# Kernel optimization log

Hardware: AMD Instinct MI355X
Metric: run time of the kernel (lower is better)

## Reference

```python
import jax, jax.numpy as jnp
import numpy as np

N, D, E, H, K = 4096, 512, 32, 128, 4  # tokens, d_model, n_experts, expert hidden, top-k


def setup_inputs() -> dict:
    key = jax.random.key(0)
    k0, k1, k2, k3 = jax.random.split(key, 4)
    x = jax.random.normal(k0, (N, D), dtype=jnp.float32)
    # router weights, init std = d**-0.5 (matches get_initializer std)
    expert_sel = jax.random.normal(k1, (E, D), dtype=jnp.float32) * (D ** -0.5)
    # per-expert MLP weights (Linear stores [out, in]; we keep [E, in, out] layout)
    w1 = jax.random.normal(k2, (E, D, H), dtype=jnp.float32) * (D ** -0.5)
    w2 = jax.random.normal(k3, (E, H, D), dtype=jnp.float32) * (H ** -0.5)
    return {"x": x, "expert_sel": expert_sel, "w1": w1, "w2": w2}


def reference(x, expert_sel, w1, w2):
    # routing: sigmoid selection, top-k experts per token
    scores = jax.nn.sigmoid(x @ expert_sel.T)          # [N, E]
    gate_vals, gate_idx = jax.lax.top_k(scores, K)     # [N, K]
    # dense gate matrix with only top-k nonzero (sparse dispatch/combine weights)
    gate = (jax.nn.one_hot(gate_idx, E, dtype=x.dtype) * gate_vals[..., None]).sum(-2)  # [N, E]
    # per-expert MLP; gating at hidden is exact since experts have no bias:
    # gate * (relu(x W1) W2) == (gate * relu(x W1)) W2
    h = jax.nn.relu(jnp.einsum('nd,edh->neh', x, w1)) * gate[..., None]  # [N, E, H]
    y = jnp.einsum('neh,ehv->nv', h, w2)               # [N, D]
    return y
```

## Files before the change

### kernel.cpp

```cpp
#include <hip/hip_runtime.h>
#include <hip/hip_bf16.h>

#define NTOK 4096
#define DM   512
#define NE   32
#define HD   128
#define TK   4

typedef unsigned short u16;
typedef unsigned int   u32;
typedef u16   u16x4 __attribute__((ext_vector_type(4)));
typedef u16   u16x8 __attribute__((ext_vector_type(8)));
typedef short short8 __attribute__((ext_vector_type(8)));
typedef float f32x4 __attribute__((ext_vector_type(4)));

__device__ __forceinline__ u16 f2bf(float f) {
    union { float f; u32 u; } v; v.f = f;
    return (u16)((v.u + 0x7FFFu + ((v.u >> 16) & 1u)) >> 16);
}
__device__ __forceinline__ float bf2f(u16 h) {
    union { u32 u; float f; } v; v.u = ((u32)h) << 16; return v.f;
}

__global__ __launch_bounds__(256) void prep_kernel(const float* __restrict__ x,
                                                   const float* __restrict__ sel,
                                                   const float* __restrict__ w1,
                                                   const float* __restrict__ w2,
                                                   int* __restrict__ counts_pad,
                                                   int* __restrict__ tok_list,
                                                   float* __restrict__ gate_list,
                                                   u16* __restrict__ xbf,
                                                   u16* __restrict__ wf1,
                                                   u16* __restrict__ wf2) {
    __shared__ float  xs[4][520];
    __shared__ double sc[4][33];
    int tid = threadIdx.x;
    int wv = tid >> 6, lane = tid & 63;

    if (blockIdx.x >= 1024) {
        int m = lane & 15, q = lane >> 4;
        int f0 = ((blockIdx.x - 1024) * 4 + wv) * 2;
        const float* in[2]; u16* outp[2]; int Nd[2];
#pragma unroll
        for (int u = 0; u < 2; ++u) {
            int w = f0 + u;
            if (w < 4096) {
                int e = w >> 7, rem = w & 127, ks = rem >> 3, nt = rem & 7;
                in[u] = w1 + (size_t)e * DM * HD + (size_t)(32 * ks + q * 8) * HD + 16 * nt + m;
                Nd[u] = HD;
                outp[u] = wf1 + (size_t)w * 512 + lane * 8;
            } else {
                int wl = w - 4096, e = wl >> 7, rem = wl & 127, ks = rem >> 5, nt = rem & 31;
                in[u] = w2 + (size_t)e * HD * DM + (size_t)(32 * ks + q * 8) * DM + 16 * nt + m;
                Nd[u] = DM;
                outp[u] = wf2 + (size_t)wl * 512 + lane * 8;
            }
        }
        float v[2][8];
#pragma unroll
        for (int u = 0; u < 2; ++u)
#pragma unroll
            for (int j = 0; j < 8; ++j) v[u][j] = in[u][(size_t)j * Nd[u]];
#pragma unroll
        for (int u = 0; u < 2; ++u) {
            u16x8 h;
#pragma unroll
            for (int j = 0; j < 8; ++j) h[j] = f2bf(v[u][j]);
            *(u16x8*)outp[u] = h;
        }
        return;
    }

    int tb = blockIdx.x * 4;
#pragma unroll
    for (int rep = 0; rep < 2; ++rep) {
        int idx = (rep * 256 + tid) * 4;
        int row = idx >> 9, col = idx & 511;
        f32x4 v = *(const f32x4*)(x + (size_t)(tb + row) * DM + col);
        *(f32x4*)&xs[row][col] = v;
        u16x4 h;
#pragma unroll
        for (int j = 0; j < 4; ++j) h[j] = f2bf(v[j]);
        *(u16x4*)(xbf + (size_t)(tb + row) * DM + col) = h;
    }
    __syncthreads();

    int tok = tid & 3, seg = (tid >> 2) & 1, e = tid >> 3;
    const float* sp = sel + (size_t)e * DM + seg * 256;
    const float* xp = &xs[tok][seg * 256];
    double pa = 0.0, pb = 0.0, pc = 0.0, pd = 0.0;
#pragma unroll 4
    for (int j = 0; j < 256; j += 16) {
        f32x4 x0 = *(const f32x4*)(xp + j);
        f32x4 x1 = *(const f32x4*)(xp + j + 4);
        f32x4 x2 = *(const f32x4*)(xp + j + 8);
        f32x4 x3 = *(const f32x4*)(xp + j + 12);
        f32x4 s0 = *(const f32x4*)(sp + j);
        f32x4 s1 = *(const f32x4*)(sp + j + 4);
        f32x4 s2 = *(const f32x4*)(sp + j + 8);
        f32x4 s3 = *(const f32x4*)(sp + j + 12);
#pragma unroll
        for (int k = 0; k < 4; ++k) {
            pa = fma((double)x0[k], (double)s0[k], pa);
            pb = fma((double)x1[k], (double)s1[k], pb);
            pc = fma((double)x2[k], (double)s2[k], pc);
            pd = fma((double)x3[k], (double)s3[k], pd);
        }
    }
    double p = (pa + pb) + (pc + pd);
    p += __shfl_xor(p, 4);
    if (seg == 0) sc[tok][e] = p;
    __syncthreads();

    if (tid < 4) {
        int t = tb + tid;
        unsigned mask = 0;
        for (int k = 0; k < TK; ++k) {
            double best = -1e300; int be = 0;
            for (int ee = 0; ee < NE; ++ee) {
                double v = sc[tid][ee];
                if (!((mask >> ee) & 1u) && v > best) { best = v; be = ee; }
            }
            mask |= 1u << be;
            float gate = 1.0f / (1.0f + __expf(-(float)best));
            int pos = atomicAdd(&counts_pad[32 * be], 1);
            tok_list[be * NTOK + pos]  = (k << 16) | t;
            gate_list[be * NTOK + pos] = gate;
        }
    }
}

__global__ __launch_bounds__(256, 2) void moe_mlp_kernel(const u16* __restrict__ xbf,
                                                         const u16* __restrict__ wf1,
                                                         const u16* __restrict__ wf2,
                                                         const int* __restrict__ counts_pad,
                                                         const int* __restrict__ tok_list,
                                                         const float* __restrict__ gate_list,
                                                         u16* __restrict__ part,
                                                         float* __restrict__ out,
                                                         int use_part) {
    __shared__ int   s_cnt[NE];
    __shared__ int   s_ent[64];
    __shared__ float s_gate[64];
    __shared__ __align__(16) u16 Hm[64][136];
    __shared__ __align__(16) u16 Ct[32][520];

    int tid = threadIdx.x;
    if (tid < NE) s_cnt[tid] = counts_pad[32 * tid];
    __syncthreads();

    int b = blockIdx.x;
    int xcd = b & 7, idx = b >> 3;
    int e = -1, t = 0, rows = 0, pre = 0;
#pragma unroll
    for (int j = 0; j < 4; ++j) {
        int ee = xcd + 8 * j;
        int cc = s_cnt[ee];
        int nt = (cc + 63) >> 6;
        if (e < 0 && idx < pre + nt) { e = ee; t = idx - pre; rows = cc - t * 64; if (rows > 64) rows = 64; }
        pre += nt;
    }
    if (e < 0) return;

    if (tid < 64) {
        int base = e * NTOK + t * 64;
        bool val = tid < rows;
        s_ent[tid]  = tok_list[base + (val ? tid : 0)];
        s_gate[tid] = val ? gate_list[base + tid] : 0.0f;
    }
    __syncthreads();

    int wv = tid >> 6, lane = tid & 63, m = lane & 15, q = lane >> 4;
    int r = wv >> 1, c = wv & 1;
    const u16* w1f = wf1 + (size_t)e * (128 * 512);
    const u16* w2f = wf2 + (size_t)e * (128 * 512);

    const u16* a0 = xbf + (size_t)(s_ent[32 * r + m] & 0xFFFF) * DM + q * 8;
    const u16* a1 = xbf + (size_t)(s_ent[32 * r + 16 + m] & 0xFFFF) * DM + q * 8;

    short8 ab[2][2][2];
    short8 bb[2][2][4];
#pragma unroll
    for (int kk = 0; kk < 2; ++kk) {
        ab[0][kk][0] = *(const short8*)(a0 + 32 * kk);
        ab[0][kk][1] = *(const short8*)(a1 + 32 * kk);
        const u16* bp = w1f + (size_t)kk * 4096 + (size_t)(4 * c) * 512 + lane * 8;
#pragma unroll
        for (int n = 0; n < 4; ++n) bb[0][kk][n] = *(const short8*)(bp + n * 512);
    }
    f32x4 acc[2][4];
#pragma unroll
    for (int i = 0; i < 2; ++i)
#pragma unroll
        for (int n = 0; n < 4; ++n) acc[i][n] = (f32x4){0.f, 0.f, 0.f, 0.f};

#pragma unroll
    for (int kp = 0; kp < 8; ++kp) {
        int cur = kp & 1, nxt = cur ^ 1;
        if (kp < 7) {
            int ks0 = 2 * (kp + 1);
#pragma unroll
            for (int kk = 0; kk < 2; ++kk) {
                ab[nxt][kk][0] = *(const short8*)(a0 + 32 * (ks0 + kk));
                ab[nxt][kk][1] = *(const short8*)(a1 + 32 * (ks0 + kk));
                const u16* bp = w1f + (size_t)(ks0 + kk) * 4096 + (size_t)(4 * c) * 512 + lane * 8;
#pragma unroll
                for (int n = 0; n < 4; ++n) bb[nxt][kk][n] = *(const short8*)(bp + n * 512);
            }
        }
#pragma unroll
        for (int kk = 0; kk < 2; ++kk)
#pragma unroll
            for (int i = 0; i < 2; ++i)
#pragma unroll
                for (int n = 0; n < 4; ++n)
                    acc[i][n] = __builtin_amdgcn_mfma_f32_16x16x32_bf16(ab[cur][kk][i],
                                                                        bb[cur][kk][n],
                                                                        acc[i][n], 0, 0, 0);
    }

#pragma unroll
    for (int i = 0; i < 2; ++i) {
        int rb = 32 * r + 16 * i + q * 4;
#pragma unroll
        for (int n = 0; n < 4; ++n)
#pragma unroll
            for (int rr = 0; rr < 4; ++rr)
                Hm[rb + rr][64 * c + 16 * n + m] =
                    f2bf(fmaxf(acc[i][n][rr], 0.f) * s_gate[rb + rr]);
    }

    short8 cb[4][8];
#pragma unroll
    for (int ks = 0; ks < 4; ++ks) {
        const u16* bp = w2f + (size_t)(ks * 32 + wv * 8) * 512 + lane * 8;
#pragma unroll
        for (int n = 0; n < 8; ++n) cb[ks][n] = *(const short8*)(bp + n * 512);
    }
    __syncthreads();

#pragma unroll
    for (int half = 0; half < 2; ++half) {
        f32x4 acc2[2][8];
#pragma unroll
        for (int i = 0; i < 2; ++i)
#pragma unroll
            for (int n = 0; n < 8; ++n) acc2[i][n] = (f32x4){0.f, 0.f, 0.f, 0.f};
#pragma unroll
        for (int ks = 0; ks < 4; ++ks) {
            short8 h0 = *(const short8*)&Hm[32 * half + m][32 * ks + q * 8];
            short8 h1 = *(const short8*)&Hm[32 * half + 16 + m][32 * ks + q * 8];
#pragma unroll
            for (int n = 0; n < 8; ++n) {
                acc2[0][n] = __builtin_amdgcn_mfma_f32_16x16x32_bf16(h0, cb[ks][n], acc2[0][n], 0, 0, 0);
                acc2[1][n] = __builtin_amdgcn_mfma_f32_16x16x32_bf16(h1, cb[ks][n], acc2[1][n], 0, 0, 0);
            }
        }
#pragma unroll
        for (int i = 0; i < 2; ++i) {
            int rb = 16 * i + q * 4;
#pragma unroll
            for (int n = 0; n < 8; ++n)
#pragma unroll
                for (int rr = 0; rr < 4; ++rr)
                    Ct[rb + rr][128 * wv + 16 * n + m] = f2bf(acc2[i][n][rr]);
        }
        __syncthreads();
#pragma unroll
        for (int rep = 0; rep < 8; ++rep) {
            int rl = rep * 4 + wv;
            int rt = 32 * half + rl;
            u16x8 v = *(const u16x8*)&Ct[rl][lane * 8];
            if (rt < rows) {
                int en = s_ent[rt];
                int tk = en & 0xFFFF, sl2 = en >> 16;
                if (use_part) {
                    *(u16x8*)(part + ((size_t)sl2 * NTOK + tk) * DM + lane * 8) = v;
                } else {
                    float* op = out + (size_t)tk * DM + lane * 8;
#pragma unroll
                    for (int j = 0; j < 8; ++j) atomicAdd(&op[j], bf2f(v[j]));
                }
            }
        }
        __syncthreads();
    }
}

__global__ __launch_bounds__(256) void combine_kernel(const u16* __restrict__ part,
                                                      float* __restrict__ out) {
    size_t off = ((size_t)blockIdx.x * 256 + threadIdx.x) * 8;
    float s[8] = {0, 0, 0, 0, 0, 0, 0, 0};
#pragma unroll
    for (int k = 0; k < TK; ++k) {
        u16x8 p = *(const u16x8*)(part + (size_t)k * NTOK * DM + off);
#pragma unroll
        for (int j = 0; j < 8; ++j) s[j] += bf2f(p[j]);
    }
    *(f32x4*)(out + off)     = (f32x4){s[0], s[1], s[2], s[3]};
    *(f32x4*)(out + off + 4) = (f32x4){s[4], s[5], s[6], s[7]};
}

extern "C" void kernel_launch(void* const* d_in, const int* in_sizes, int n_in,
                              void* d_out, int out_size, void* d_ws, size_t ws_size,
                              hipStream_t stream) {
    const float* x   = (const float*)d_in[0];
    const float* sel = (const float*)d_in[1];
    const float* w1  = (const float*)d_in[2];
    const float* w2  = (const float*)d_in[3];
    float* out = (float*)d_out;

    char* ws = (char*)d_ws;
    int*   counts_pad = (int*)(ws);
    int*   tok_list   = (int*)(ws + 4096);
    float* gate_list  = (float*)(ws + 4096 + (size_t)NE * NTOK * 4);
    u16*   xbf  = (u16*)(ws + 4096 + (size_t)NE * NTOK * 8);
    u16*   wf1  = xbf + (size_t)NTOK * DM;
    u16*   wf2  = wf1 + (size_t)NE * HD * DM;
    u16*   part = wf2 + (size_t)NE * HD * DM;

    size_t need = 4096 + (size_t)NE * NTOK * 8 + (size_t)NTOK * DM * 2
                + 2 * (size_t)NE * HD * DM * 2 + (size_t)TK * NTOK * DM * 2;
    int use_part = (ws_size >= need) ? 1 : 0;

    hipMemsetAsync(counts_pad, 0, 4096, stream);
    if (!use_part)
        hipMemsetAsync(d_out, 0, (size_t)NTOK * DM * sizeof(float), stream);

    prep_kernel<<<2048, 256, 0, stream>>>(x, sel, w1, w2, counts_pad, tok_list,
                                          gate_list, xbf, wf1, wf2);
    moe_mlp_kernel<<<2080, 256, 0, stream>>>(xbf, wf1, wf2, counts_pad, tok_list,
                                             gate_list, part, out, use_part);
    if (use_part)
        combine_kernel<<<NTOK * DM / 8 / 256, 256, 0, stream>>>(part, out);
}
```

Baseline: 120.5 us.

## Halve MoE token tile to 32 rows and double-buffer W2 loads

Each block of the expert MLP kernel now handles 32 routed tokens instead of 64, and the grid doubles to 4096 blocks. The goal is less padding waste per expert and more blocks to spread across CUs. The second GEMM now streams W2 fragments through a two-slot register buffer instead of preloading all four k-slices, which cuts register pressure. In exchange, each expert's W1/W2 weights are reloaded twice as often per token, so global weight traffic rises.

```diff
diff --git a/kernel.cpp b/kernel.cpp
--- a/kernel.cpp
+++ b/kernel.cpp
@@ -140,9 +140,9 @@
                                                          float* __restrict__ out,
                                                          int use_part) {
     __shared__ int   s_cnt[NE];
-    __shared__ int   s_ent[64];
-    __shared__ float s_gate[64];
-    __shared__ __align__(16) u16 Hm[64][136];
+    __shared__ int   s_ent[32];
+    __shared__ float s_gate[32];
+    __shared__ __align__(16) u16 Hm[32][136];
     __shared__ __align__(16) u16 Ct[32][520];
 
     int tid = threadIdx.x;
@@ -156,14 +156,14 @@
     for (int j = 0; j < 4; ++j) {
         int ee = xcd + 8 * j;
         int cc = s_cnt[ee];
-        int nt = (cc + 63) >> 6;
-        if (e < 0 && idx < pre + nt) { e = ee; t = idx - pre; rows = cc - t * 64; if (rows > 64) rows = 64; }
+        int nt = (cc + 31) >> 5;
+        if (e < 0 && idx < pre + nt) { e = ee; t = idx - pre; rows = cc - t * 32; if (rows > 32) rows = 32; }
         pre += nt;
     }
     if (e < 0) return;
 
-    if (tid < 64) {
-        int base = e * NTOK + t * 64;
+    if (tid < 32) {
+        int base = e * NTOK + t * 32;
         bool val = tid < rows;
         s_ent[tid]  = tok_list[base + (val ? tid : 0)];
         s_gate[tid] = val ? gate_list[base + tid] : 0.0f;
@@ -175,24 +175,20 @@
     const u16* w1f = wf1 + (size_t)e * (128 * 512);
     const u16* w2f = wf2 + (size_t)e * (128 * 512);
 
-    const u16* a0 = xbf + (size_t)(s_ent[32 * r + m] & 0xFFFF) * DM + q * 8;
-    const u16* a1 = xbf + (size_t)(s_ent[32 * r + 16 + m] & 0xFFFF) * DM + q * 8;
-
-    short8 ab[2][2][2];
+    const u16* a0 = xbf + (size_t)(s_ent[16 * r + m] & 0xFFFF) * DM + q * 8;
+
+    short8 ab[2][2];
     short8 bb[2][2][4];
 #pragma unroll
     for (int kk = 0; kk < 2; ++kk) {
-        ab[0][kk][0] = *(const short8*)(a0 + 32 * kk);
-        ab[0][kk][1] = *(const short8*)(a1 + 32 * kk);
+        ab[0][kk] = *(const short8*)(a0 + 32 * kk);
         const u16* bp = w1f + (size_t)kk * 4096 + (size_t)(4 * c) * 512 + lane * 8;
 #pragma unroll
         for (int n = 0; n < 4; ++n) bb[0][kk][n] = *(const short8*)(bp + n * 512);
     }
-    f32x4 acc[2][4];
-#pragma unroll
-    for (int i = 0; i < 2; ++i)
-#pragma unroll
-        for (int n = 0; n < 4; ++n) acc[i][n] = (f32x4){0.f, 0.f, 0.f, 0.f};
+    f32x4 acc[4];
+#pragma unroll
+    for (int n = 0; n < 4; ++n) acc[n] = (f32x4){0.f, 0.f, 0.f, 0.f};
 
 #pragma unroll
     for (int kp = 0; kp < 8; ++kp) {
@@ -201,8 +197,7 @@
             int ks0 = 2 * (kp + 1);
 #pragma unroll
             for (int kk = 0; kk < 2; ++kk) {
-                ab[nxt][kk][0] = *(const short8*)(a0 + 32 * (ks0 + kk));
-                ab[nxt][kk][1] = *(const short8*)(a1 + 32 * (ks0 + kk));
+                ab[nxt][kk] = *(const short8*)(a0 + 32 * (ks0 + kk));
                 const u16* bp = w1f + (size_t)(ks0 + kk) * 4096 + (size_t)(4 * c) * 512 + lane * 8;
 #pragma unroll
                 for (int n = 0; n < 4; ++n) bb[nxt][kk][n] = *(const short8*)(bp + n * 512);
@@ -211,79 +206,77 @@
 #pragma unroll
         for (int kk = 0; kk < 2; ++kk)
 #pragma unroll
-            for (int i = 0; i < 2; ++i)
-#pragma unroll
-                for (int n = 0; n < 4; ++n)
-                    acc[i][n] = __builtin_amdgcn_mfma_f32_16x16x32_bf16(ab[cur][kk][i],
-                                                                        bb[cur][kk][n],
-                                                                        acc[i][n], 0, 0, 0);
-    }
-
-#pragma unroll
-    for (int i = 0; i < 2; ++i) {
-        int rb = 32 * r + 16 * i + q * 4;
+            for (int n = 0; n < 4; ++n)
+                acc[n] = __builtin_amdgcn_mfma_f32_16x16x32_bf16(ab[cur][kk],
+                                                                 bb[cur][kk][n],
+                                                                 acc[n], 0, 0, 0);
+    }
+
+    {
+        int rb = 16 * r + q * 4;
 #pragma unroll
         for (int n = 0; n < 4; ++n)
 #pragma unroll
             for (int rr = 0; rr < 4; ++rr)
                 Hm[rb + rr][64 * c + 16 * n + m] =
-                    f2bf(fmaxf(acc[i][n][rr], 0.f) * s_gate[rb + rr]);
-    }
-
-    short8 cb[4][8];
+                    f2bf(fmaxf(acc[n][rr], 0.f) * s_gate[rb + rr]);
+    }
+
+    short8 cb[2][8];
+    {
+        const u16* bp = w2f + (size_t)(wv * 8) * 512 + lane * 8;
+#pragma unroll
+        for (int n = 0; n < 8; ++n) cb[0][n] = *(const short8*)(bp + n * 512);
+    }
+    __syncthreads();
+
+    f32x4 acc2[2][8];
+#pragma unroll
+    for (int i = 0; i < 2; ++i)
+#pragma unroll
+        for (int n = 0; n < 8; ++n) acc2[i][n] = (f32x4){0.f, 0.f, 0.f, 0.f};
 #pragma unroll
     for (int ks = 0; ks < 4; ++ks) {
-        const u16* bp = w2f + (size_t)(ks * 32 + wv * 8) * 512 + lane * 8;
-#pragma unroll
-        for (int n = 0; n < 8; ++n) cb[ks][n] = *(const short8*)(bp + n * 512);
-    }
-    __syncthreads();
-
-#pragma unroll
-    for (int half = 0; half < 2; ++half) {
-        f32x4 acc2[2][8];
-#pragma unroll
-        for (int i = 0; i < 2; ++i)
-#pragma unroll
-            for (int n = 0; n < 8; ++n) acc2[i][n] = (f32x4){0.f, 0.f, 0.f, 0.f};
-#pragma unroll
-        for (int ks = 0; ks < 4; ++ks) {
-            short8 h0 = *(const short8*)&Hm[32 * half + m][32 * ks + q * 8];
-            short8 h1 = *(const short8*)&Hm[32 * half + 16 + m][32 * ks + q * 8];
-#pragma unroll
-            for (int n = 0; n < 8; ++n) {
-                acc2[0][n] = __builtin_amdgcn_mfma_f32_16x16x32_bf16(h0, cb[ks][n], acc2[0][n], 0, 0, 0);
-                acc2[1][n] = __builtin_amdgcn_mfma_f32_16x16x32_bf16(h1, cb[ks][n], acc2[1][n], 0, 0, 0);
+        int cur = ks & 1, nxt = cur ^ 1;
+        if (ks < 3) {
+            const u16* bp = w2f + (size_t)((ks + 1) * 32 + wv * 8) * 512 + lane * 8;
+#pragma unroll
+            for (int n = 0; n < 8; ++n) cb[nxt][n] = *(const short8*)(bp + n * 512);
+        }
+        short8 h0 = *(const short8*)&Hm[m][32 * ks + q * 8];
+        short8 h1 = *(const short8*)&Hm[16 + m][32 * ks + q * 8];
+#pragma unroll
+        for (int n = 0; n < 8; ++n) {
+            acc2[0][n] = __builtin_amdgcn_mfma_f32_16x16x32_bf16(h0, cb[cur][n], acc2[0][n], 0, 0, 0);
+            acc2[1][n] = __builtin_amdgcn_mfma_f32_16x16x32_bf16(h1, cb[cur][n], acc2[1][n], 0, 0, 0);
+        }
+    }
+
+#pragma unroll
+    for (int i = 0; i < 2; ++i) {
+        int rb = 16 * i + q * 4;
+#pragma unroll
+        for (int n = 0; n < 8; ++n)
+#pragma unroll
+            for (int rr = 0; rr < 4; ++rr)
+                Ct[rb + rr][128 * wv + 16 * n + m] = f2bf(acc2[i][n][rr]);
+    }
+    __syncthreads();
+#pragma unroll
+    for (int rep = 0; rep < 8; ++rep) {
+        int rl = rep * 4 + wv;
+        u16x8 v = *(const u16x8*)&Ct[rl][lane * 8];
+        if (rl < rows) {
+            int en = s_ent[rl];
+            int tk = en & 0xFFFF, sl2 = en >> 16;
+            if (use_part) {
+                *(u16x8*)(part + ((size_t)sl2 * NTOK + tk) * DM + lane * 8) = v;
+            } else {
+                float* op = out + (size_t)tk * DM + lane * 8;
+#pragma unroll
+                for (int j = 0; j < 8; ++j) atomicAdd(&op[j], bf2f(v[j]));
             }
         }
-#pragma unroll
-        for (int i = 0; i < 2; ++i) {
-            int rb = 16 * i + q * 4;
-#pragma unroll
-            for (int n = 0; n < 8; ++n)
-#pragma unroll
-                for (int rr = 0; rr < 4; ++rr)
-                    Ct[rb + rr][128 * wv + 16 * n + m] = f2bf(acc2[i][n][rr]);
-        }
-        __syncthreads();
-#pragma unroll
-        for (int rep = 0; rep < 8; ++rep) {
-            int rl = rep * 4 + wv;
-            int rt = 32 * half + rl;
-            u16x8 v = *(const u16x8*)&Ct[rl][lane * 8];
-            if (rt < rows) {
-                int en = s_ent[rt];
-                int tk = en & 0xFFFF, sl2 = en >> 16;
-                if (use_part) {
-                    *(u16x8*)(part + ((size_t)sl2 * NTOK + tk) * DM + lane * 8) = v;
-                } else {
-                    float* op = out + (size_t)tk * DM + lane * 8;
-#pragma unroll
-                    for (int j = 0; j < 8; ++j) atomicAdd(&op[j], bf2f(v[j]));
-                }
-            }
-        }
-        __syncthreads();
     }
 }
 
@@ -329,7 +322,7 @@
 
     prep_kernel<<<2048, 256, 0, stream>>>(x, sel, w1, w2, counts_pad, tok_list,
                                           gate_list, xbf, wf1, wf2);
-    moe_mlp_kernel<<<2080, 256, 0, stream>>>(xbf, wf1, wf2, counts_pad, tok_list,
+    moe_mlp_kernel<<<4096, 256, 0, stream>>>(xbf, wf1, wf2, counts_pad, tok_list,
                                              gate_list, part, out, use_part);
     if (use_part)
         combine_kernel<<<NTOK * DM / 8 / 256, 256, 0, stream>>>(part, out);
```

Measured after the change: 117.7 us. -2.3%, faster.
